# Performance work log

Measured on AMD Instinct MI355X. Metric: run time of the kernel, lower is better.

## Reference

```python
import jax, jax.numpy as jnp
import numpy as np
import math

N = 100000      # num nodes
D = 5           # fixed degree per node (<=5 -> exact Shapley enumeration path)
F_IN = 128
F_OUT = 128


def _subset_coeffs(d):
    """Exact Shapley subset-enumeration coefficients for a node with d neighbors.
    For subset S (mask m_k over neighbor slots, |S|=s):
      marginal = (sum_S + x_i)/(s+1) - (sum_S/s if s>0 else 0)   [since mean_S]
      weight   = s! (d-s)! / (d+1)!
    contrib = sum_k w_k*marginal_k = einsum(sum_S, c1) + x_i * sum(c2)
    """
    k = np.arange(2 ** d)
    masks = ((k[:, None] >> np.arange(d)) & 1).astype(np.float32)  # [2^d, d]
    s = masks.sum(axis=1)
    fact = np.vectorize(math.factorial)
    w = (fact(s.astype(np.int64)) * fact((d - s).astype(np.int64))
         / math.factorial(d + 1)).astype(np.float32)
    c1 = np.where(s > 0, w * (1.0 / (s + 1.0) - 1.0 / np.maximum(s, 1.0)), 0.0).astype(np.float32)
    c2 = (w / (s + 1.0)).astype(np.float32)
    return jnp.asarray(masks), jnp.asarray(c1), jnp.asarray(float(c2.sum()))


def setup_inputs() -> dict:
    key = jax.random.key(0)
    k1, k2, k3 = jax.random.split(key, 3)
    x = jax.random.normal(k1, (N, F_IN), dtype=jnp.float32)
    # fixed-degree graph: node i owns edges [i*D, (i+1)*D); row sorted
    row = jnp.repeat(jnp.arange(N, dtype=jnp.int32), D)
    col = jax.random.randint(k2, (N * D,), 0, N, dtype=jnp.int32)
    edge_index = jnp.stack([row, col])  # [2, N*D]
    W = jax.random.normal(k3, (F_OUT, F_IN), dtype=jnp.float32) / np.float32(np.sqrt(F_IN))
    return {"x": x, "edge_index": edge_index, "W": W}


def reference(x, edge_index, W):
    n = x.shape[0]
    col = edge_index[1]
    d = col.shape[0] // n
    nbrs = col.reshape(n, d)          # neighbors of node i (row is sorted, fixed degree)
    xn = x[nbrs]                      # [n, d, f] gathered neighbor features
    masks, c1, c2_sum = _subset_coeffs(d)
    # per-subset neighbor-feature sums: [n, 2^d, f]
    sum_S = jnp.einsum('kd,ndf->nkf', masks, xn)
    contrib = jnp.einsum('nkf,k->nf', sum_S, c1) + x * c2_sum
    shapley = x + contrib             # x_i + Shapley contribution
    out = jax.nn.relu(shapley @ W.T)  # Linear(bias=False) + relu
    return out
```

## Files before the change

kernel.cpp:

```cpp
#include <hip/hip_runtime.h>
#include <hip/hip_bf16.h>

typedef __attribute__((ext_vector_type(8))) short short8;
typedef __attribute__((ext_vector_type(4))) float f32x4;
typedef __attribute__((ext_vector_type(2))) unsigned u32x2;

#define DEG 5
#define FDIM 128
#define MT 64
#define NTHR 256
#define LROW 136

#define CSELF 1.4083333333333334f
#define ALPHA (-0.04833333333333333f)

__device__ __forceinline__ short f2bf(float f) {
    unsigned u = __builtin_bit_cast(unsigned, f);
    unsigned r = (u + 0x7fffu + ((u >> 16) & 1u)) >> 16;
    return (short)(r & 0xffffu);
}
__device__ __forceinline__ float bf2f(short s) {
    return __builtin_bit_cast(float, (unsigned)((unsigned short)s) << 16);
}

__device__ __forceinline__ unsigned f32_to_fp8(float x) {
    unsigned u = __builtin_bit_cast(unsigned, x);
    unsigned s = (u >> 24) & 0x80u;
    unsigned t = u & 0x7FFFFFFFu;
    unsigned r = t + 0x7FFFFu + ((t >> 20) & 1u);
    unsigned em = (r >> 20);
    em = (em < 968u) ? 0u : (em - 960u);
    return s | (em & 0x7Fu);
}
__device__ __forceinline__ float fp8_to_f32(unsigned b) {
    unsigned s = (b & 0x80u) << 24;
    unsigned em = b & 0x7Fu;
    unsigned f = s | ((em + 960u) << 20);
    return (em < 8u) ? __builtin_bit_cast(float, s) : __builtin_bit_cast(float, f);
}

__global__ __launch_bounds__(256) void prep_w_kernel(
    const float* __restrict__ W, short* __restrict__ wswz)
{
    int t = blockIdx.x * 256 + threadIdx.x;
    int frag = t >> 6;
    int lane = t & 63;
    int tt = frag >> 2;
    int kk = frag & 3;
    int lr = lane & 15;
    int lg = lane >> 4;
    const float4* wp = reinterpret_cast<const float4*>(W + (tt * 16 + lr) * FDIM + kk * 32 + lg * 8);
    float4 w0 = wp[0], w1 = wp[1];
    short8 v;
    v[0] = f2bf(w0.x); v[1] = f2bf(w0.y); v[2] = f2bf(w0.z); v[3] = f2bf(w0.w);
    v[4] = f2bf(w1.x); v[5] = f2bf(w1.y); v[6] = f2bf(w1.z); v[7] = f2bf(w1.w);
    *reinterpret_cast<short8*>(wswz + (size_t)t * 8) = v;
}

__global__ __launch_bounds__(NTHR) void gemm_y_kernel(
    const float* __restrict__ x,
    const short* __restrict__ wswz,
    short* __restrict__ Y,
    unsigned char* __restrict__ Y8,
    int n)
{
    __shared__ short sS[MT * LROW];
    const int tid = threadIdx.x;
    const int base = blockIdx.x * MT;

    for (int t = tid; t < MT * 16; t += NTHR) {
        int m = t >> 4;
        int c = t & 15;
        int node = base + m;
        short8 v;
        if (node < n) {
            const f32x4* xp = reinterpret_cast<const f32x4*>(x + (size_t)node * FDIM + c * 8);
            f32x4 s0 = __builtin_nontemporal_load(xp);
            f32x4 s1 = __builtin_nontemporal_load(xp + 1);
            v[0] = f2bf(s0[0]); v[1] = f2bf(s0[1]); v[2] = f2bf(s0[2]); v[3] = f2bf(s0[3]);
            v[4] = f2bf(s1[0]); v[5] = f2bf(s1[1]); v[6] = f2bf(s1[2]); v[7] = f2bf(s1[3]);
        } else {
            v = (short8)0;
        }
        *reinterpret_cast<short8*>(&sS[m * LROW + c * 8]) = v;
    }
    __syncthreads();

    const int wave = tid >> 6;
    const int lane = tid & 63;
    const int lr = lane & 15;
    const int lg = lane >> 4;

    short8 afrag[4];
    const short* arow = &sS[(wave * 16 + lr) * LROW];
    #pragma unroll
    for (int kk = 0; kk < 4; ++kk)
        afrag[kk] = *reinterpret_cast<const short8*>(arow + kk * 32 + lg * 8);
    __syncthreads();

    f32x4 acc[8];
    #pragma unroll
    for (int t = 0; t < 8; ++t) acc[t] = (f32x4){0.f, 0.f, 0.f, 0.f};

    #pragma unroll
    for (int t = 0; t < 8; ++t) {
        #pragma unroll
        for (int kk = 0; kk < 4; ++kk) {
            short8 bfrag = *reinterpret_cast<const short8*>(
                wswz + (((size_t)(t * 4 + kk) * 64 + lane) * 8));
            acc[t] = __builtin_amdgcn_mfma_f32_16x16x32_bf16(afrag[kk], bfrag, acc[t], 0, 0, 0);
        }
    }

    #pragma unroll
    for (int t = 0; t < 8; ++t) {
        #pragma unroll
        for (int i = 0; i < 4; ++i) {
            sS[(wave * 16 + lg * 4 + i) * LROW + t * 16 + lr] = f2bf(acc[t][i]);
        }
    }
    __syncthreads();

    for (int t = tid; t < MT * 16; t += NTHR) {
        int m = t >> 4;
        int c = t & 15;
        int node = base + m;
        if (node < n) {
            short8 v = *reinterpret_cast<const short8*>(&sS[m * LROW + c * 8]);
            *reinterpret_cast<short8*>(Y + (size_t)node * FDIM + c * 8) = v;
            unsigned d0 = 0, d1 = 0;
            #pragma unroll
            for (int k = 0; k < 4; ++k)
                d0 |= f32_to_fp8(bf2f(v[k])) << (8 * k);
            #pragma unroll
            for (int k = 0; k < 4; ++k)
                d1 |= f32_to_fp8(bf2f(v[4 + k])) << (8 * k);
            u32x2 pk; pk[0] = d0; pk[1] = d1;
            *reinterpret_cast<u32x2*>(Y8 + (size_t)node * FDIM + c * 8) = pk;
        }
    }
}

__global__ __launch_bounds__(NTHR) void combine_kernel(
    const short* __restrict__ Y,
    const unsigned char* __restrict__ Y8,
    const int* __restrict__ col,
    float* __restrict__ out,
    int n)
{
    __shared__ int sIdx[MT * DEG];
    const int tid = threadIdx.x;
    const int base = blockIdx.x * MT;

    for (int i = tid; i < MT * DEG; i += NTHR) {
        int e = base * DEG + i;
        sIdx[i] = (e < n * DEG) ? col[e] : 0;
    }
    __syncthreads();

    const int slot = tid >> 4;
    const int c = tid & 15;

    u32x2 g[4][DEG];
    short8 sv[4];

    #pragma unroll
    for (int u = 0; u < 4; ++u) {
        int ms = u * 16 + slot;
        int node = base + ms;
        int nc = node < n ? node : 0;
        sv[u] = *reinterpret_cast<const short8*>(Y + (size_t)nc * FDIM + c * 8);
        #pragma unroll
        for (int j = 0; j < DEG; ++j) {
            int nb = sIdx[ms * DEG + j];
            g[u][j] = *reinterpret_cast<const u32x2*>(Y8 + (size_t)nb * FDIM + c * 8);
        }
    }

    #pragma unroll
    for (int u = 0; u < 4; ++u) {
        int node = base + u * 16 + slot;
        if (node < n) {
            float r[8];
            #pragma unroll
            for (int k = 0; k < 8; ++k) {
                unsigned sh = 8 * (k & 3);
                float s = 0.f;
                #pragma unroll
                for (int j = 0; j < DEG; ++j) {
                    unsigned w = (k < 4) ? g[u][j][0] : g[u][j][1];
                    s += fp8_to_f32((w >> sh) & 0xFFu);
                }
                float v = CSELF * bf2f(sv[u][k]) + ALPHA * s;
                r[k] = v > 0.f ? v : 0.f;
            }
            f32x4* op = reinterpret_cast<f32x4*>(out + (size_t)node * FDIM + c * 8);
            __builtin_nontemporal_store((f32x4){r[0], r[1], r[2], r[3]}, op);
            __builtin_nontemporal_store((f32x4){r[4], r[5], r[6], r[7]}, op + 1);
        }
    }
}

__global__ __launch_bounds__(NTHR) void shapley_gnn_kernel(
    const float* __restrict__ x,
    const int* __restrict__ col,
    const short* __restrict__ wswz,
    float* __restrict__ out,
    int n)
{
    __shared__ short sS[MT * LROW];
    __shared__ int sIdx[MT * DEG];

    const int tid = threadIdx.x;
    const int base = blockIdx.x * MT;

    for (int i = tid; i < MT * DEG; i += NTHR) {
        int e = base * DEG + i;
        sIdx[i] = (e < n * DEG) ? col[e] : 0;
    }
    __syncthreads();

    for (int t = tid; t < MT * 16; t += NTHR) {
        int m = t >> 4;
        int c = t & 15;
        int node = base + m;
        float a0, a1, a2, a3, a4, a5, a6, a7;
        if (node < n) {
            const float4* xp = reinterpret_cast<const float4*>(x + (size_t)node * FDIM + c * 8);
            float4 s0 = xp[0], s1 = xp[1];
            a0 = CSELF * s0.x; a1 = CSELF * s0.y; a2 = CSELF * s0.z; a3 = CSELF * s0.w;
            a4 = CSELF * s1.x; a5 = CSELF * s1.y; a6 = CSELF * s1.z; a7 = CSELF * s1.w;
            #pragma unroll
            for (int j = 0; j < DEG; ++j) {
                int nb = sIdx[m * DEG + j];
                const float4* np = reinterpret_cast<const float4*>(x + (size_t)nb * FDIM + c * 8);
                float4 b0 = np[0], b1 = np[1];
                a0 += ALPHA * b0.x; a1 += ALPHA * b0.y; a2 += ALPHA * b0.z; a3 += ALPHA * b0.w;
                a4 += ALPHA * b1.x; a5 += ALPHA * b1.y; a6 += ALPHA * b1.z; a7 += ALPHA * b1.w;
            }
        } else {
            a0 = a1 = a2 = a3 = a4 = a5 = a6 = a7 = 0.f;
        }
        short8 v;
        v[0] = f2bf(a0); v[1] = f2bf(a1); v[2] = f2bf(a2); v[3] = f2bf(a3);
        v[4] = f2bf(a4); v[5] = f2bf(a5); v[6] = f2bf(a6); v[7] = f2bf(a7);
        *reinterpret_cast<short8*>(&sS[m * LROW + c * 8]) = v;
    }
    __syncthreads();

    const int wave = tid >> 6;
    const int lane = tid & 63;
    const int lr = lane & 15;
    const int lg = lane >> 4;

    short8 afrag[4];
    const short* arow = &sS[(wave * 16 + lr) * LROW];
    #pragma unroll
    for (int kk = 0; kk < 4; ++kk)
        afrag[kk] = *reinterpret_cast<const short8*>(arow + kk * 32 + lg * 8);

    f32x4 acc[8];
    #pragma unroll
    for (int t = 0; t < 8; ++t) acc[t] = (f32x4){0.f, 0.f, 0.f, 0.f};

    #pragma unroll
    for (int t = 0; t < 8; ++t) {
        #pragma unroll
        for (int kk = 0; kk < 4; ++kk) {
            short8 bfrag = *reinterpret_cast<const short8*>(
                wswz + (((size_t)(t * 4 + kk) * 64 + lane) * 8));
            acc[t] = __builtin_amdgcn_mfma_f32_16x16x32_bf16(afrag[kk], bfrag, acc[t], 0, 0, 0);
        }
    }

    #pragma unroll
    for (int t = 0; t < 8; ++t) {
        #pragma unroll
        for (int i = 0; i < 4; ++i) {
            int nrow = base + wave * 16 + lg * 4 + i;
            if (nrow < n) {
                float v = acc[t][i];
                out[(size_t)nrow * FDIM + t * 16 + lr] = v > 0.f ? v : 0.f;
            }
        }
    }
}

extern "C" void kernel_launch(void* const* d_in, const int* in_sizes, int n_in,
                              void* d_out, int out_size, void* d_ws, size_t ws_size,
                              hipStream_t stream) {
    const float* x  = (const float*)d_in[0];
    const int* ei   = (const int*)d_in[1];
    const float* W  = (const float*)d_in[2];
    float* out      = (float*)d_out;

    int n = in_sizes[0] / FDIM;
    const int* col = ei + (size_t)n * DEG;

    short* wswz = (short*)d_ws;
    size_t y_off  = 32768;
    size_t y_sz   = (size_t)n * FDIM * sizeof(short);
    size_t y8_off = (y_off + y_sz + 255) & ~(size_t)255;
    size_t need   = y8_off + (size_t)n * FDIM;

    hipLaunchKernelGGL(prep_w_kernel, dim3(8), dim3(256), 0, stream, W, wswz);

    int blocks = (n + MT - 1) / MT;
    if (ws_size >= need) {
        short* Y          = (short*)((char*)d_ws + y_off);
        unsigned char* Y8 = (unsigned char*)d_ws + y8_off;
        hipLaunchKernelGGL(gemm_y_kernel, dim3(blocks), dim3(NTHR), 0, stream,
                           x, wswz, Y, Y8, n);
        hipLaunchKernelGGL(combine_kernel, dim3(blocks), dim3(NTHR), 0, stream,
                           Y, Y8, col, out, n);
    } else {
        hipLaunchKernelGGL(shapley_gnn_kernel, dim3(blocks), dim3(NTHR), 0, stream,
                           x, col, wswz, out, n);
    }
}
```

Baseline: 62.09 us.

## Aggregate fp8 neighbor features before GEMM instead of after

```diff
diff --git a/kernel.cpp b/kernel.cpp
--- a/kernel.cpp
+++ b/kernel.cpp
@@ -57,98 +57,33 @@
     *reinterpret_cast<short8*>(wswz + (size_t)t * 8) = v;
 }
 
-__global__ __launch_bounds__(NTHR) void gemm_y_kernel(
+__global__ __launch_bounds__(256) void conv_x8_kernel(
+    const float* __restrict__ x, unsigned char* __restrict__ x8, long total8)
+{
+    long t = (long)blockIdx.x * 256 + threadIdx.x;
+    if (t < total8) {
+        const f32x4* xp = reinterpret_cast<const f32x4*>(x + t * 8);
+        f32x4 a = xp[0], b = xp[1];
+        unsigned d0 = f32_to_fp8(a[0]) | (f32_to_fp8(a[1]) << 8)
+                    | (f32_to_fp8(a[2]) << 16) | (f32_to_fp8(a[3]) << 24);
+        unsigned d1 = f32_to_fp8(b[0]) | (f32_to_fp8(b[1]) << 8)
+                    | (f32_to_fp8(b[2]) << 16) | (f32_to_fp8(b[3]) << 24);
+        u32x2 pk; pk[0] = d0; pk[1] = d1;
+        *reinterpret_cast<u32x2*>(x8 + t * 8) = pk;
+    }
+}
+
+__global__ __launch_bounds__(NTHR) void shapley_gnn_kernel(
     const float* __restrict__ x,
+    const unsigned char* __restrict__ x8,
+    const int* __restrict__ col,
     const short* __restrict__ wswz,
-    short* __restrict__ Y,
-    unsigned char* __restrict__ Y8,
-    int n)
-{
-    __shared__ short sS[MT * LROW];
-    const int tid = threadIdx.x;
-    const int base = blockIdx.x * MT;
-
-    for (int t = tid; t < MT * 16; t += NTHR) {
-        int m = t >> 4;
-        int c = t & 15;
-        int node = base + m;
-        short8 v;
-        if (node < n) {
-            const f32x4* xp = reinterpret_cast<const f32x4*>(x + (size_t)node * FDIM + c * 8);
-            f32x4 s0 = __builtin_nontemporal_load(xp);
-            f32x4 s1 = __builtin_nontemporal_load(xp + 1);
-            v[0] = f2bf(s0[0]); v[1] = f2bf(s0[1]); v[2] = f2bf(s0[2]); v[3] = f2bf(s0[3]);
-            v[4] = f2bf(s1[0]); v[5] = f2bf(s1[1]); v[6] = f2bf(s1[2]); v[7] = f2bf(s1[3]);
-        } else {
-            v = (short8)0;
-        }
-        *reinterpret_cast<short8*>(&sS[m * LROW + c * 8]) = v;
-    }
-    __syncthreads();
-
-    const int wave = tid >> 6;
-    const int lane = tid & 63;
-    const int lr = lane & 15;
-    const int lg = lane >> 4;
-
-    short8 afrag[4];
-    const short* arow = &sS[(wave * 16 + lr) * LROW];
-    #pragma unroll
-    for (int kk = 0; kk < 4; ++kk)
-        afrag[kk] = *reinterpret_cast<const short8*>(arow + kk * 32 + lg * 8);
-    __syncthreads();
-
-    f32x4 acc[8];
-    #pragma unroll
-    for (int t = 0; t < 8; ++t) acc[t] = (f32x4){0.f, 0.f, 0.f, 0.f};
-
-    #pragma unroll
-    for (int t = 0; t < 8; ++t) {
-        #pragma unroll
-        for (int kk = 0; kk < 4; ++kk) {
-            short8 bfrag = *reinterpret_cast<const short8*>(
-                wswz + (((size_t)(t * 4 + kk) * 64 + lane) * 8));
-            acc[t] = __builtin_amdgcn_mfma_f32_16x16x32_bf16(afrag[kk], bfrag, acc[t], 0, 0, 0);
-        }
-    }
-
-    #pragma unroll
-    for (int t = 0; t < 8; ++t) {
-        #pragma unroll
-        for (int i = 0; i < 4; ++i) {
-            sS[(wave * 16 + lg * 4 + i) * LROW + t * 16 + lr] = f2bf(acc[t][i]);
-        }
-    }
-    __syncthreads();
-
-    for (int t = tid; t < MT * 16; t += NTHR) {
-        int m = t >> 4;
-        int c = t & 15;
-        int node = base + m;
-        if (node < n) {
-            short8 v = *reinterpret_cast<const short8*>(&sS[m * LROW + c * 8]);
-            *reinterpret_cast<short8*>(Y + (size_t)node * FDIM + c * 8) = v;
-            unsigned d0 = 0, d1 = 0;
-            #pragma unroll
-            for (int k = 0; k < 4; ++k)
-                d0 |= f32_to_fp8(bf2f(v[k])) << (8 * k);
-            #pragma unroll
-            for (int k = 0; k < 4; ++k)
-                d1 |= f32_to_fp8(bf2f(v[4 + k])) << (8 * k);
-            u32x2 pk; pk[0] = d0; pk[1] = d1;
-            *reinterpret_cast<u32x2*>(Y8 + (size_t)node * FDIM + c * 8) = pk;
-        }
-    }
-}
-
-__global__ __launch_bounds__(NTHR) void combine_kernel(
-    const short* __restrict__ Y,
-    const unsigned char* __restrict__ Y8,
-    const int* __restrict__ col,
     float* __restrict__ out,
     int n)
 {
+    __shared__ short sS[MT * LROW];
     __shared__ int sIdx[MT * DEG];
+
     const int tid = threadIdx.x;
     const int base = blockIdx.x * MT;
 
@@ -161,27 +96,29 @@
     const int slot = tid >> 4;
     const int c = tid & 15;
 
+    f32x4 xs[4][2];
     u32x2 g[4][DEG];
-    short8 sv[4];
-
     #pragma unroll
     for (int u = 0; u < 4; ++u) {
         int ms = u * 16 + slot;
         int node = base + ms;
         int nc = node < n ? node : 0;
-        sv[u] = *reinterpret_cast<const short8*>(Y + (size_t)nc * FDIM + c * 8);
+        const f32x4* xp = reinterpret_cast<const f32x4*>(x + (size_t)nc * FDIM + c * 8);
+        xs[u][0] = xp[0];
+        xs[u][1] = xp[1];
         #pragma unroll
         for (int j = 0; j < DEG; ++j) {
             int nb = sIdx[ms * DEG + j];
-            g[u][j] = *reinterpret_cast<const u32x2*>(Y8 + (size_t)nb * FDIM + c * 8);
+            g[u][j] = *reinterpret_cast<const u32x2*>(x8 + (size_t)nb * FDIM + c * 8);
         }
     }
 
     #pragma unroll
     for (int u = 0; u < 4; ++u) {
-        int node = base + u * 16 + slot;
+        int ms = u * 16 + slot;
+        int node = base + ms;
+        short8 v;
         if (node < n) {
-            float r[8];
             #pragma unroll
             for (int k = 0; k < 8; ++k) {
                 unsigned sh = 8 * (k & 3);
@@ -191,17 +128,55 @@
                     unsigned w = (k < 4) ? g[u][j][0] : g[u][j][1];
                     s += fp8_to_f32((w >> sh) & 0xFFu);
                 }
-                float v = CSELF * bf2f(sv[u][k]) + ALPHA * s;
-                r[k] = v > 0.f ? v : 0.f;
-            }
-            f32x4* op = reinterpret_cast<f32x4*>(out + (size_t)node * FDIM + c * 8);
-            __builtin_nontemporal_store((f32x4){r[0], r[1], r[2], r[3]}, op);
-            __builtin_nontemporal_store((f32x4){r[4], r[5], r[6], r[7]}, op + 1);
-        }
-    }
-}
-
-__global__ __launch_bounds__(NTHR) void shapley_gnn_kernel(
+                float xv = (k < 4) ? xs[u][0][k & 3] : xs[u][1][k & 3];
+                v[k] = f2bf(CSELF * xv + ALPHA * s);
+            }
+        } else {
+            v = (short8)0;
+        }
+        *reinterpret_cast<short8*>(&sS[ms * LROW + c * 8]) = v;
+    }
+    __syncthreads();
+
+    const int wave = tid >> 6;
+    const int lane = tid & 63;
+    const int lr = lane & 15;
+    const int lg = lane >> 4;
+
+    short8 afrag[4];
+    const short* arow = &sS[(wave * 16 + lr) * LROW];
+    #pragma unroll
+    for (int kk = 0; kk < 4; ++kk)
+        afrag[kk] = *reinterpret_cast<const short8*>(arow + kk * 32 + lg * 8);
+
+    f32x4 acc[8];
+    #pragma unroll
+    for (int t = 0; t < 8; ++t) acc[t] = (f32x4){0.f, 0.f, 0.f, 0.f};
+
+    #pragma unroll
+    for (int t = 0; t < 8; ++t) {
+        #pragma unroll
+        for (int kk = 0; kk < 4; ++kk) {
+            short8 bfrag = *reinterpret_cast<const short8*>(
+                wswz + (((size_t)(t * 4 + kk) * 64 + lane) * 8));
+            acc[t] = __builtin_amdgcn_mfma_f32_16x16x32_bf16(afrag[kk], bfrag, acc[t], 0, 0, 0);
+        }
+    }
+
+    #pragma unroll
+    for (int t = 0; t < 8; ++t) {
+        #pragma unroll
+        for (int i = 0; i < 4; ++i) {
+            int nrow = base + wave * 16 + lg * 4 + i;
+            if (nrow < n) {
+                float v = acc[t][i];
+                out[(size_t)nrow * FDIM + t * 16 + lr] = v > 0.f ? v : 0.f;
+            }
+        }
+    }
+}
+
+__global__ __launch_bounds__(NTHR) void shapley_fb_kernel(
     const float* __restrict__ x,
     const int* __restrict__ col,
     const short* __restrict__ wswz,
@@ -298,23 +273,22 @@
     const int* col = ei + (size_t)n * DEG;
 
     short* wswz = (short*)d_ws;
-    size_t y_off  = 32768;
-    size_t y_sz   = (size_t)n * FDIM * sizeof(short);
-    size_t y8_off = (y_off + y_sz + 255) & ~(size_t)255;
-    size_t need   = y8_off + (size_t)n * FDIM;
+    size_t x8_off = 32768;
+    size_t need   = x8_off + (size_t)n * FDIM;
 
     hipLaunchKernelGGL(prep_w_kernel, dim3(8), dim3(256), 0, stream, W, wswz);
 
     int blocks = (n + MT - 1) / MT;
     if (ws_size >= need) {
-        short* Y          = (short*)((char*)d_ws + y_off);
-        unsigned char* Y8 = (unsigned char*)d_ws + y8_off;
-        hipLaunchKernelGGL(gemm_y_kernel, dim3(blocks), dim3(NTHR), 0, stream,
-                           x, wswz, Y, Y8, n);
-        hipLaunchKernelGGL(combine_kernel, dim3(blocks), dim3(NTHR), 0, stream,
-                           Y, Y8, col, out, n);
+        unsigned char* x8 = (unsigned char*)d_ws + x8_off;
+        long total8 = (long)n * FDIM / 8;
+        int cblocks = (int)((total8 + 255) / 256);
+        hipLaunchKernelGGL(conv_x8_kernel, dim3(cblocks), dim3(256), 0, stream,
+                           x, x8, total8);
+        hipLaunchKernelGGL(shapley_gnn_kernel, dim3(blocks), dim3(NTHR), 0, stream,
+                           x, x8, col, wswz, out, n);
     } else {
-        hipLaunchKernelGGL(shapley_gnn_kernel, dim3(blocks), dim3(NTHR), 0, stream,
+        hipLaunchKernelGGL(shapley_fb_kernel, dim3(blocks), dim3(NTHR), 0, stream,
                            x, col, wswz, out, n);
     }
 }
```

Result: faster. 56.20 us (-9.5%).
